# Optimization experiments

Measured on AMD Instinct MI355X. Metric: run time of the kernel, lower is better.

## Reference

```python
import jax, jax.numpy as jnp
import numpy as np

N = 50000      # nodes
E = 1600000    # edges
R = 12         # relations (num_unique_edge_attrs)
F_IN = 64      # num_node_features
H = 128        # hidden_channels
C = 10         # num_classes
G = 256        # graphs in batch
EPS = 1e-5     # BatchNorm eps


def setup_inputs() -> dict:
    key = jax.random.key(0)
    ks = jax.random.split(key, 10)
    s = 0.05
    return {
        "x": jax.random.normal(ks[0], (N, F_IN), jnp.float32),
        "Wrel1": jax.random.normal(ks[1], (R, F_IN, H), jnp.float32) * s,
        "root1": jax.random.normal(ks[2], (F_IN, H), jnp.float32) * s,
        "bias1": jnp.zeros((H,), jnp.float32),
        "gamma1": jnp.ones((H,), jnp.float32),
        "beta1": jnp.zeros((H,), jnp.float32),
        "Wrel2": jax.random.normal(ks[3], (R, H, H), jnp.float32) * s,
        "root2": jax.random.normal(ks[4], (H, H), jnp.float32) * s,
        "bias2": jnp.zeros((H,), jnp.float32),
        "gamma2": jnp.ones((H,), jnp.float32),
        "beta2": jnp.zeros((H,), jnp.float32),
        "Wf": jax.random.normal(ks[5], (H, C), jnp.float32) * s,
        "bf": jnp.zeros((C,), jnp.float32),
        "edge_index": jax.random.randint(ks[6], (2, E), 0, N, dtype=jnp.int64) if jax.config.jax_enable_x64 else jax.random.randint(ks[6], (2, E), 0, N),
        "edge_type": jax.random.randint(ks[7], (E,), 0, R),
        "batch": jnp.sort(jax.random.randint(ks[8], (N,), 0, G)),
    }


def _segment_mean(vals, idx, num):
    # mean aggregation; empty segments -> 0
    s = jax.ops.segment_sum(vals, idx, num_segments=num)
    c = jax.ops.segment_sum(jnp.ones(idx.shape, vals.dtype), idx, num_segments=num)
    return s / jnp.clip(c, 1.0)[:, None]


def _rgcn(x, Wrel, root, bias, src, dst, edge_type):
    # PyG RGCNConv with aggr='mean': per-relation mean of source features, then W_r
    seg = dst * R + edge_type                      # fused (node, relation) segment id
    h = _segment_mean(x[src], seg, N * R)          # [N*R, in]
    h = h.reshape(N, R, x.shape[1])
    return jnp.einsum('nri,rio->no', h, Wrel) + x @ root + bias


def _bn(x, gamma, beta):
    # BatchNorm1d training-mode math (batch statistics, biased variance)
    mu = jnp.mean(x, axis=0)
    var = jnp.mean((x - mu) ** 2, axis=0)
    return gamma * (x - mu) / jnp.sqrt(var + EPS) + beta


def reference(x, Wrel1, root1, bias1, gamma1, beta1,
              Wrel2, root2, bias2, gamma2, beta2,
              Wf, bf, edge_index, edge_type, batch):
    src, dst = edge_index[0], edge_index[1]
    h = jax.nn.relu(_bn(_rgcn(x, Wrel1, root1, bias1, src, dst, edge_type), gamma1, beta1))
    h = jax.nn.relu(_bn(_rgcn(h, Wrel2, root2, bias2, src, dst, edge_type), gamma2, beta2))
    pooled = _segment_mean(h, batch, G)            # global_mean_pool -> [G, H]
    return pooled @ Wf + bf                        # [G, C]
```

## Files before the change

### kernel.cpp

```cpp
#include <hip/hip_runtime.h>

constexpr int N_NODES = 50000;
constexpr int N_EDGES = 1600000;
constexpr int NREL    = 12;
constexpr int F_INPUT = 64;
constexpr int HID     = 128;
constexpr int NCLS    = 10;
constexpr int NGRAPH  = 256;
constexpr int NSEG    = N_NODES * NREL;
constexpr float BN_EPS = 1e-5f;

constexpr int NB    = 391;
constexpr int SEGB  = 128 * NREL;
constexpr int NBLK  = 392;
constexpr int PTPB  = 1024;
constexpr int EPB   = 4096;

typedef float v4f __attribute__((ext_vector_type(4)));
typedef short s8b __attribute__((ext_vector_type(8)));

__device__ __forceinline__ unsigned f2bf(float f) {
    unsigned u = __float_as_uint(f);
    return (u + 0x7FFFu + ((u >> 16) & 1u)) >> 16;
}
__device__ __forceinline__ unsigned pack2(float a, float b) {
    return f2bf(a) | (f2bf(b) << 16);
}

constexpr int PQ0 = 64;
constexpr int PQ1 = PQ0 + 64;
constexpr int PQ2 = PQ1 + 8192;
constexpr int PQ3 = PQ2 + 13 * F_INPUT * HID;
constexpr int PQ4 = PQ3 + 13 * HID * HID;
constexpr int PQ5 = PQ4 + N_NODES * F_INPUT / 4;
constexpr int PQ6 = PQ5 + NGRAPH;
constexpr int PREP_BLOCKS = (PQ6 + 255) / 256;

__global__ void prep(const float* __restrict__ Wrel1, const float* __restrict__ root1,
                     const float* __restrict__ Wrel2, const float* __restrict__ root2,
                     const float* __restrict__ x, const int* __restrict__ batch,
                     ushort* __restrict__ Wp1, ushort* __restrict__ Wp2,
                     ushort* __restrict__ xb,
                     float* __restrict__ bn1, float* __restrict__ bn2,
                     float* __restrict__ psum, float* __restrict__ pcnt) {
    int tid = blockIdx.x * 256 + threadIdx.x;
    const uint4 z = make_uint4(0, 0, 0, 0);
    if (tid < PQ0) { reinterpret_cast<uint4*>(bn1)[tid] = z; return; }
    if (tid < PQ1) { reinterpret_cast<uint4*>(bn2)[tid - PQ0] = z; return; }
    if (tid < PQ2) { reinterpret_cast<uint4*>(psum)[tid - PQ1] = z; return; }
    if (tid < PQ3) {
        int idx = tid - PQ2;
        int r = idx >> 13, rem = idx & 8191;
        int k = rem >> 7, n = rem & 127;
        const float* W = (r < NREL) ? (Wrel1 + (size_t)r * 8192) : root1;
        float v = W[k * HID + n];
        int b = k >> 5, kk = k & 31;
        int j = (n & 7) * 16 + (n >> 3);
        Wp1[(((size_t)(r * 2 + b)) * HID + j) * 32 + kk] = (ushort)f2bf(v);
        return;
    }
    if (tid < PQ4) {
        int idx = tid - PQ3;
        int r = idx >> 14, rem = idx & 16383;
        int k = rem >> 7, n = rem & 127;
        const float* W = (r < NREL) ? (Wrel2 + (size_t)r * 16384) : root2;
        float v = W[k * HID + n];
        int b = k >> 5, kk = k & 31;
        int j = (n & 7) * 16 + (n >> 3);
        Wp2[(((size_t)(r * 4 + b)) * HID + j) * 32 + kk] = (ushort)f2bf(v);
        return;
    }
    if (tid < PQ5) {
        int i = tid - PQ4;
        float4 v = reinterpret_cast<const float4*>(x)[i];
        uint2 o;
        o.x = pack2(v.x, v.y);
        o.y = pack2(v.z, v.w);
        reinterpret_cast<uint2*>(xb)[i] = o;
        return;
    }
    if (tid < PQ6) {
        int g = tid - PQ5;
        int lo0 = 0, hi0 = N_NODES;
        while (lo0 < hi0) { int m = (lo0 + hi0) >> 1; if (batch[m] < g) lo0 = m + 1; else hi0 = m; }
        int lo1 = lo0, hi1 = N_NODES;
        while (lo1 < hi1) { int m = (lo1 + hi1) >> 1; if (batch[m] < g + 1) lo1 = m + 1; else hi1 = m; }
        pcnt[g] = (float)(lo1 - lo0);
    }
}


__global__ __launch_bounds__(PTPB)
void part_hist(const int* __restrict__ dst, int* __restrict__ histG) {
    __shared__ int h[NB];
    int t = threadIdx.x, blk = blockIdx.x;
    if (t < NB) h[t] = 0;
    __syncthreads();
    int base = blk * EPB;
#pragma unroll
    for (int it = 0; it < EPB / PTPB; ++it) {
        int e = base + it * PTPB + t;
        if (e < N_EDGES) atomicAdd(&h[dst[e] >> 7], 1);
    }
    __syncthreads();
    if (t < NB) histG[blk * NB + t] = h[t];
}

__global__ __launch_bounds__(512)
void part_scanA(const int* __restrict__ histG, int* __restrict__ cursorG,
                int* __restrict__ bucketTot) {
    __shared__ int s[512];
    int t = threadIdx.x, b = blockIdx.x;
    int v = (t < NBLK) ? histG[t * NB + b] : 0;
    s[t] = v;
    __syncthreads();
    for (int d = 1; d < 512; d <<= 1) {
        int x = (t >= d) ? s[t - d] : 0;
        __syncthreads();
        s[t] += x;
        __syncthreads();
    }
    if (t < NBLK) cursorG[t * NB + b] = s[t] - v;
    if (t == NBLK - 1) bucketTot[b] = s[t];
}

__global__ __launch_bounds__(512)
void part_scanB(const int* __restrict__ bucketTot, int* __restrict__ bucketBase) {
    __shared__ int s[512];
    int t = threadIdx.x;
    int v = (t < NB) ? bucketTot[t] : 0;
    s[t] = v;
    __syncthreads();
    for (int d = 1; d < 512; d <<= 1) {
        int x = (t >= d) ? s[t - d] : 0;
        __syncthreads();
        s[t] += x;
        __syncthreads();
    }
    if (t <= NB) bucketBase[t] = (t == 0) ? 0 : s[t - 1];
}

__global__ __launch_bounds__(PTPB)
void part_scatter(const int* __restrict__ src, const int* __restrict__ dst,
                  const int* __restrict__ et, const int* __restrict__ cursorG,
                  const int* __restrict__ bucketBase, uint* __restrict__ ebuck) {
    __shared__ int cur[NB];
    int t = threadIdx.x, blk = blockIdx.x;
    if (t < NB) cur[t] = cursorG[blk * NB + t] + bucketBase[t];
    __syncthreads();
    int base = blk * EPB;
#pragma unroll
    for (int it = 0; it < EPB / PTPB; ++it) {
        int e = base + it * PTPB + t;
        if (e < N_EDGES) {
            int d = dst[e];
            int b = d >> 7;
            int pos = atomicAdd(&cur[b], 1);
            ebuck[pos] = (uint)src[e] | ((uint)(d & 127) << 16) | ((uint)et[e] << 23);
        }
    }
}

__global__ __launch_bounds__(256)
void csr_finalize(const uint* __restrict__ ebuck, const int* __restrict__ bucketBase,
                  int* __restrict__ off, int* __restrict__ zrow, float* __restrict__ wgt) {
    __shared__ int cnt[SEGB];
    __shared__ int cur[SEGB];
    __shared__ float winv[SEGB];
    __shared__ int partial[256];
    int t = threadIdx.x, b = blockIdx.x;
    int eb0 = bucketBase[b], eb1 = bucketBase[b + 1];
#pragma unroll
    for (int i = 0; i < 6; ++i) cnt[t * 6 + i] = 0;
    __syncthreads();
    for (int e = eb0 + t; e < eb1; e += 256) {
        uint u = ebuck[e];
        int key = (int)((u >> 16) & 127) * NREL + (int)(u >> 23);
        atomicAdd(&cnt[key], 1);
    }
    __syncthreads();
    int loc[6];
    int sum = 0;
#pragma unroll
    for (int i = 0; i < 6; ++i) { loc[i] = sum; sum += cnt[t * 6 + i]; }
    partial[t] = sum;
    __syncthreads();
    for (int d = 1; d < 256; d <<= 1) {
        int v = (t >= d) ? partial[t - d] : 0;
        __syncthreads();
        partial[t] += v;
        __syncthreads();
    }
    int tbase = (t == 0) ? 0 : partial[t - 1];
    int nodeb = b * 128;
#pragma unroll
    for (int i = 0; i < 6; ++i) {
        int s = t * 6 + i;
        int gpos = eb0 + tbase + loc[i];
        cur[s] = gpos;
        int c = cnt[s];
        winv[s] = (c > 0) ? 1.0f / (float)c : 0.f;
        int node = nodeb + s / NREL;
        if (node < N_NODES) off[node * NREL + (s % NREL)] = gpos;
    }
    __syncthreads();
    for (int e = eb0 + t; e < eb1; e += 256) {
        uint u = ebuck[e];
        int rel = (int)(u >> 23);
        int key = (int)((u >> 16) & 127) * NREL + rel;
        int pos = atomicAdd(&cur[key], 1);
        zrow[pos] = rel * N_NODES + (int)(u & 0xFFFFu);
        wgt[pos] = winv[key];
    }
    if (b == 0 && t == 0) off[NSEG] = N_EDGES;
}


__device__ __constant__ int REL_SPLIT[5] = {0, 4, 7, 10, 13};

template <int F>
__launch_bounds__(256)
__global__ void gemm_rel(const ushort* __restrict__ xin, const ushort* __restrict__ Wp,
                         ushort* __restrict__ Z) {
    constexpr int TN  = 128;
    constexpr int FP2 = F + 8;
    constexpr int KB  = F / 32;
    constexpr int CHW = F / 4;
    constexpr int NLD = CHW / 8;
    __shared__ __align__(16) ushort A[TN * FP2];
    const int t = threadIdx.x;
    const int n0 = blockIdx.x * TN;
    const int r0 = REL_SPLIT[blockIdx.y], r1 = REL_SPLIT[blockIdx.y + 1];
    const int lane = t & 63, wave = t >> 6, q = lane >> 4, l16 = lane & 15;

    {
        const int nl = t >> 2, tid4 = t & 3;
#pragma unroll
        for (int g = 0; g < 2; ++g) {
            int row = g * 64 + nl;
            int n = n0 + row;
            uint4* dstp = reinterpret_cast<uint4*>(A + row * FP2 + tid4 * CHW);
            if (n < N_NODES) {
                const uint4* srcp =
                    reinterpret_cast<const uint4*>(xin + (size_t)n * F + tid4 * CHW);
#pragma unroll
                for (int c = 0; c < NLD; ++c) dstp[c] = srcp[c];
            } else {
                uint4 zz = make_uint4(0, 0, 0, 0);
#pragma unroll
                for (int c = 0; c < NLD; ++c) dstp[c] = zz;
            }
        }
    }
    __syncthreads();

    const int rowbase = wave * 32;
    for (int rel = r0; rel < r1; ++rel) {
        v4f acc[2][8];
#pragma unroll
        for (int st = 0; st < 2; ++st)
#pragma unroll
            for (int nt = 0; nt < 8; ++nt) acc[st][nt] = (v4f){0.f, 0.f, 0.f, 0.f};
#pragma unroll
        for (int b = 0; b < KB; ++b) {
            s8b bfr[8];
            const ushort* wb = Wp + ((size_t)(rel * KB + b) * HID + l16) * 32 + q * 8;
#pragma unroll
            for (int nt = 0; nt < 8; ++nt)
                bfr[nt] = *reinterpret_cast<const s8b*>(wb + (size_t)nt * 16 * 32);
#pragma unroll
            for (int st = 0; st < 2; ++st) {
                s8b af = *reinterpret_cast<const s8b*>(
                    A + (rowbase + st * 16 + l16) * FP2 + b * 32 + q * 8);
#pragma unroll
                for (int nt = 0; nt < 8; ++nt)
                    acc[st][nt] =
                        __builtin_amdgcn_mfma_f32_16x16x32_bf16(af, bfr[nt], acc[st][nt], 0, 0, 0);
            }
        }
        ushort* zr = Z + (size_t)rel * ((size_t)N_NODES * HID);
#pragma unroll
        for (int st = 0; st < 2; ++st) {
            int rowb = n0 + rowbase + st * 16 + q * 4;
#pragma unroll
            for (int rr = 0; rr < 4; ++rr) {
                int n = rowb + rr;
                if (n < N_NODES) {
                    uint4 o;
                    o.x = pack2(acc[st][0][rr], acc[st][1][rr]);
                    o.y = pack2(acc[st][2][rr], acc[st][3][rr]);
                    o.z = pack2(acc[st][4][rr], acc[st][5][rr]);
                    o.w = pack2(acc[st][6][rr], acc[st][7][rr]);
                    *reinterpret_cast<uint4*>(zr + (size_t)n * HID + l16 * 8) = o;
                }
            }
        }
    }
}


__launch_bounds__(256)
__global__ void agg_bn(const ushort* __restrict__ Z, const int* __restrict__ off,
                       const int* __restrict__ zrow, const float* __restrict__ wgt,
                       const float* __restrict__ bias,
                       float* __restrict__ H, float* __restrict__ bn_sum,
                       float* __restrict__ bn_sq) {
    __shared__ float RED[2][4][HID];
    const int t = threadIdx.x;
    const int lane = t & 63, wave = t >> 6;
    const int n0 = blockIdx.x * 32 + wave * 8;
    const float2 bv = *reinterpret_cast<const float2*>(bias + lane * 2);
    float ps0 = 0.f, ps1 = 0.f, pq0 = 0.f, pq1 = 0.f;

    for (int i = 0; i < 8; ++i) {
        int n = n0 + i;
        if (n >= N_NODES) break;
        int e0 = off[n * NREL];
        int ee = off[n * NREL + NREL];
        uint ur = *reinterpret_cast<const uint*>(
            Z + ((size_t)12 * N_NODES + n) * HID + lane * 2);
        float a0 = __uint_as_float(ur << 16) + bv.x;
        float a1 = __uint_as_float(ur & 0xFFFF0000u) + bv.y;
        int elast = ee - 1;
        for (int e = e0; e < ee; e += 8) {
            int zr_[8];
            float w_[8];
#pragma unroll
            for (int j = 0; j < 8; ++j) {
                int ec = min(e + j, elast);
                zr_[j] = zrow[ec];
                w_[j] = (e + j < ee) ? wgt[ec] : 0.f;
            }
            uint u_[8];
#pragma unroll
            for (int j = 0; j < 8; ++j)
                u_[j] = *reinterpret_cast<const uint*>(
                    Z + (size_t)zr_[j] * HID + lane * 2);
#pragma unroll
            for (int j = 0; j < 8; ++j) {
                a0 += __uint_as_float(u_[j] << 16) * w_[j];
                a1 += __uint_as_float(u_[j] & 0xFFFF0000u) * w_[j];
            }
        }
        *reinterpret_cast<float2*>(H + (size_t)n * HID + lane * 2) = make_float2(a0, a1);
        ps0 += a0; ps1 += a1;
        pq0 += a0 * a0; pq1 += a1 * a1;
    }
    RED[0][wave][lane * 2] = ps0; RED[0][wave][lane * 2 + 1] = ps1;
    RED[1][wave][lane * 2] = pq0; RED[1][wave][lane * 2 + 1] = pq1;
    __syncthreads();
    {
        int stat = t >> 7, col = t & 127;
        float v = RED[stat][0][col] + RED[stat][1][col] +
                  RED[stat][2][col] + RED[stat][3][col];
        if (stat == 0) atomicAdd(&bn_sum[col], v);
        else           atomicAdd(&bn_sq[col], v);
    }
}


__global__ void bn_relu_bf16(const float* __restrict__ h, const float* __restrict__ bn_sum,
                             const float* __restrict__ bn_sq, const float* __restrict__ gamma,
                             const float* __restrict__ beta, ushort* __restrict__ outb) {
    __shared__ float CA[HID], CB[HID];
    int t = threadIdx.x;
    if (t < HID) {
        float mu = bn_sum[t] * (1.0f / N_NODES);
        float var = bn_sq[t] * (1.0f / N_NODES) - mu * mu;
        float a = gamma[t] / sqrtf(var + BN_EPS);
        CA[t] = a;
        CB[t] = beta[t] - a * mu;
    }
    __syncthreads();
    int i = blockIdx.x * 256 + t;
    constexpr int TOTAL = N_NODES * HID / 4;
    if (i < TOTAL) {
        int o4 = i & 31;
        float4 a = reinterpret_cast<const float4*>(CA)[o4];
        float4 b = reinterpret_cast<const float4*>(CB)[o4];
        float4 v = reinterpret_cast<const float4*>(h)[i];
        v.x = fmaxf(a.x * v.x + b.x, 0.f);
        v.y = fmaxf(a.y * v.y + b.y, 0.f);
        v.z = fmaxf(a.z * v.z + b.z, 0.f);
        v.w = fmaxf(a.w * v.w + b.w, 0.f);
        uint2 o;
        o.x = pack2(v.x, v.y);
        o.y = pack2(v.z, v.w);
        reinterpret_cast<uint2*>(outb)[i] = o;
    }
}


__global__ void pool_bnrelu(const float* __restrict__ h, const float* __restrict__ bn_sum,
                            const float* __restrict__ bn_sq, const float* __restrict__ gamma,
                            const float* __restrict__ beta, const int* __restrict__ batch,
                            float* __restrict__ psum) {
    __shared__ float CA[HID], CB[HID];
    int t = threadIdx.x;
    if (t < HID) {
        float mu = bn_sum[t] * (1.0f / N_NODES);
        float var = bn_sq[t] * (1.0f / N_NODES) - mu * mu;
        float a = gamma[t] / sqrtf(var + BN_EPS);
        CA[t] = a;
        CB[t] = beta[t] - a * mu;
    }
    __syncthreads();
    int col = t & 127;
    int nb = blockIdx.x * 16 + (t >> 7) * 8;
    float a = CA[col], b = CB[col];
    float run = 0.f;
    int curg = -1;
    for (int i = 0; i < 8; ++i) {
        int n = nb + i;
        if (n < N_NODES) {
            int g = batch[n];
            float v = fmaxf(a * h[(size_t)n * HID + col] + b, 0.f);
            if (g != curg) {
                if (curg >= 0) atomicAdd(&psum[curg * HID + col], run);
                run = 0.f;
                curg = g;
            }
            run += v;
        }
    }
    if (curg >= 0) atomicAdd(&psum[curg * HID + col], run);
}

__global__ void final_kernel(const float* __restrict__ psum, const float* __restrict__ pcnt,
                             const float* __restrict__ Wf, const float* __restrict__ bf,
                             float* __restrict__ out) {
    __shared__ float p[HID];
    int g = blockIdx.x, t = threadIdx.x;
    float inv = 1.0f / fmaxf(pcnt[g], 1.0f);
    p[t] = psum[g * HID + t] * inv;
    p[t + 64] = psum[g * HID + t + 64] * inv;
    __syncthreads();
    if (t < NCLS) {
        float s = bf[t];
#pragma unroll 16
        for (int k = 0; k < HID; ++k) s += p[k] * Wf[k * NCLS + t];
        out[g * NCLS + t] = s;
    }
}


extern "C" void kernel_launch(void* const* d_in, const int* in_sizes, int n_in,
                              void* d_out, int out_size, void* d_ws, size_t ws_size,
                              hipStream_t stream) {
    const float* x      = (const float*)d_in[0];
    const float* Wrel1  = (const float*)d_in[1];
    const float* root1  = (const float*)d_in[2];
    const float* bias1  = (const float*)d_in[3];
    const float* gamma1 = (const float*)d_in[4];
    const float* beta1  = (const float*)d_in[5];
    const float* Wrel2  = (const float*)d_in[6];
    const float* root2  = (const float*)d_in[7];
    const float* bias2  = (const float*)d_in[8];
    const float* gamma2 = (const float*)d_in[9];
    const float* beta2  = (const float*)d_in[10];
    const float* Wf     = (const float*)d_in[11];
    const float* bf     = (const float*)d_in[12];
    const int* ei       = (const int*)d_in[13];
    const int* et       = (const int*)d_in[14];
    const int* batch    = (const int*)d_in[15];
    const int* srcv = ei;
    const int* dstv = ei + N_EDGES;

    char* w = (char*)d_ws;
    auto alloc = [&](size_t bytes) -> char* {
        char* p = w;
        w += (bytes + 255) / 256 * 256;
        return p;
    };
    int* off     = (int*)alloc((size_t)(NSEG + 1) * 4);
    int* zrow    = (int*)alloc((size_t)N_EDGES * 4);
    float* wgt   = (float*)alloc((size_t)N_EDGES * 4);
    ushort* xb   = (ushort*)alloc((size_t)N_NODES * F_INPUT * 2);
    ushort* H1b  = (ushort*)alloc((size_t)N_NODES * HID * 2);
    ushort* Wp1  = (ushort*)alloc((size_t)13 * F_INPUT * HID * 2);
    ushort* Wp2  = (ushort*)alloc((size_t)13 * HID * HID * 2);
    float* bn1   = (float*)alloc(2 * HID * 4);
    float* bn2   = (float*)alloc(2 * HID * 4);
    float* psum  = (float*)alloc((size_t)NGRAPH * HID * 4);
    float* pcnt  = (float*)alloc((size_t)NGRAPH * 4);
    float* Hbuf  = (float*)alloc((size_t)N_NODES * HID * 4);
    char* ovl    = alloc((size_t)13 * N_NODES * HID * 2);
    int* histG      = (int*)ovl;
    int* cursorG    = (int*)(ovl + (size_t)NBLK * NB * 4);
    int* bucketTot  = (int*)(ovl + (size_t)2 * NBLK * NB * 4);
    int* bucketBase = (int*)(ovl + (size_t)2 * NBLK * NB * 4 + (NB + 1) * 4 + 252);
    uint* ebuck     = (uint*)(ovl + (size_t)2 * NBLK * NB * 4 + 4096);
    ushort* Zb      = (ushort*)ovl;

    prep<<<PREP_BLOCKS, 256, 0, stream>>>(Wrel1, root1, Wrel2, root2, x, batch,
                                          Wp1, Wp2, xb, bn1, bn2, psum, pcnt);

    part_hist<<<NBLK, PTPB, 0, stream>>>(dstv, histG);
    part_scanA<<<NB, 512, 0, stream>>>(histG, cursorG, bucketTot);
    part_scanB<<<1, 512, 0, stream>>>(bucketTot, bucketBase);
    part_scatter<<<NBLK, PTPB, 0, stream>>>(srcv, dstv, et, cursorG, bucketBase, ebuck);
    csr_finalize<<<NB, 256, 0, stream>>>(ebuck, bucketBase, off, zrow, wgt);

    dim3 ggrid((N_NODES + 127) / 128, 4);
    int ablk = (N_NODES + 31) / 32;

    gemm_rel<F_INPUT><<<ggrid, 256, 0, stream>>>(xb, Wp1, Zb);
    agg_bn<<<ablk, 256, 0, stream>>>(Zb, off, zrow, wgt, bias1, Hbuf, bn1, bn1 + HID);
    bn_relu_bf16<<<(N_NODES * HID / 4 + 255) / 256, 256, 0, stream>>>(Hbuf, bn1, bn1 + HID,
                                                                      gamma1, beta1, H1b);

    gemm_rel<HID><<<ggrid, 256, 0, stream>>>(H1b, Wp2, Zb);
    agg_bn<<<ablk, 256, 0, stream>>>(Zb, off, zrow, wgt, bias2, Hbuf, bn2, bn2 + HID);

    pool_bnrelu<<<(N_NODES + 15) / 16, 256, 0, stream>>>(Hbuf, bn2, bn2 + HID, gamma2, beta2,
                                                         batch, psum);
    final_kernel<<<NGRAPH, 64, 0, stream>>>(psum, pcnt, Wf, bf, (float*)d_out);
}
```

Measured before the change: 492.2 us.

## Aggregate-then-transform for layer 1 via per-relation mean and concatenated GEMM

For the first RGCN layer, the order of operations is swapped: the per-relation mean of 64-wide bf16 source features is computed first into a concatenated [N, 13*64] buffer (including the root self features). A single GEMM against the stacked weights then fuses bias and the BatchNorm statistic reductions. This avoids materializing and gathering the 13x128-wide transformed Z tensor, shrinking the gather width from 128 to 64. The cost is an extra esrc array written in CSR finalize and an intermediate M buffer round-trip.

```diff
diff --git a/kernel.cpp b/kernel.cpp
--- a/kernel.cpp
+++ b/kernel.cpp
@@ -163,7 +163,8 @@
 
 __global__ __launch_bounds__(256)
 void csr_finalize(const uint* __restrict__ ebuck, const int* __restrict__ bucketBase,
-                  int* __restrict__ off, int* __restrict__ zrow, float* __restrict__ wgt) {
+                  int* __restrict__ off, int* __restrict__ esrc,
+                  int* __restrict__ zrow, float* __restrict__ wgt) {
     __shared__ int cnt[SEGB];
     __shared__ int cur[SEGB];
     __shared__ float winv[SEGB];
@@ -209,10 +210,154 @@
         int rel = (int)(u >> 23);
         int key = (int)((u >> 16) & 127) * NREL + rel;
         int pos = atomicAdd(&cur[key], 1);
-        zrow[pos] = rel * N_NODES + (int)(u & 0xFFFFu);
+        int srcn = (int)(u & 0xFFFFu);
+        esrc[pos] = srcn;
+        zrow[pos] = rel * N_NODES + srcn;
         wgt[pos] = winv[key];
     }
     if (b == 0 && t == 0) off[NSEG] = N_EDGES;
+}
+
+
+template <int F>
+__launch_bounds__(256)
+__global__ void agg_m(const ushort* __restrict__ xin, const int* __restrict__ off,
+                      const int* __restrict__ esrc, ushort* __restrict__ Mb) {
+    constexpr int KT = 13 * F;
+    const int t = threadIdx.x;
+    const int lane = t & 63, wave = t >> 6;
+    const int half = lane >> 5;
+    const int cofs = (F == 128) ? lane * 2 : (lane & 31) * 2;
+    const int n0 = blockIdx.x * 32 + wave * 8;
+
+    for (int i = 0; i < 8; ++i) {
+        int n = n0 + i;
+        if (n >= N_NODES) break;
+        if (F == 128 || half == 0) {
+            uint ur = *reinterpret_cast<const uint*>(xin + (size_t)n * F + cofs);
+            *reinterpret_cast<uint*>(Mb + (size_t)n * KT + 12 * F + cofs) = ur;
+        }
+        constexpr int NR = (F == 128) ? 12 : 6;
+#pragma unroll 2
+        for (int rr = 0; rr < NR; ++rr) {
+            int r = (F == 128) ? rr : rr * 2 + half;
+            int e0 = off[n * NREL + r], e1 = off[n * NREL + r + 1];
+            float f0 = 0.f, f1 = 0.f;
+            int elast = e1 - 1;
+            for (int e = e0; e < e1; e += 4) {
+                int i0 = esrc[e];
+                int i1 = esrc[min(e + 1, elast)];
+                int i2 = esrc[min(e + 2, elast)];
+                int i3 = esrc[min(e + 3, elast)];
+                uint u0 = *reinterpret_cast<const uint*>(xin + (size_t)i0 * F + cofs);
+                uint u1 = *reinterpret_cast<const uint*>(xin + (size_t)i1 * F + cofs);
+                uint u2 = *reinterpret_cast<const uint*>(xin + (size_t)i2 * F + cofs);
+                uint u3 = *reinterpret_cast<const uint*>(xin + (size_t)i3 * F + cofs);
+                f0 += __uint_as_float(u0 << 16);
+                f1 += __uint_as_float(u0 & 0xFFFF0000u);
+                if (e + 1 < e1) { f0 += __uint_as_float(u1 << 16); f1 += __uint_as_float(u1 & 0xFFFF0000u); }
+                if (e + 2 < e1) { f0 += __uint_as_float(u2 << 16); f1 += __uint_as_float(u2 & 0xFFFF0000u); }
+                if (e + 3 < e1) { f0 += __uint_as_float(u3 << 16); f1 += __uint_as_float(u3 & 0xFFFF0000u); }
+            }
+            if (e1 > e0) {
+                float inv = 1.0f / (float)(e1 - e0);
+                f0 *= inv; f1 *= inv;
+            }
+            *reinterpret_cast<uint*>(Mb + (size_t)n * KT + r * F + cofs) = pack2(f0, f1);
+        }
+    }
+}
+
+
+template <int F>
+__launch_bounds__(256)
+__global__ void gemm_cat(const ushort* __restrict__ Mb, const ushort* __restrict__ Wp,
+                         const float* __restrict__ bias, float* __restrict__ H,
+                         float* __restrict__ bn_sum, float* __restrict__ bn_sq) {
+    constexpr int KT  = 13 * F;
+    constexpr int NCH = KT / 64;
+    __shared__ __align__(16) ushort As[64 * 72];
+    const int t = threadIdx.x;
+    const int n0 = blockIdx.x * 64;
+    const int lane = t & 63, wave = t >> 6, q = lane >> 4, l16 = lane & 15;
+    const int srow = t >> 2, sq = t & 3;
+    const int nstage = n0 + srow;
+
+    v4f acc[8];
+#pragma unroll
+    for (int nt = 0; nt < 8; ++nt) acc[nt] = (v4f){0.f, 0.f, 0.f, 0.f};
+
+    for (int c = 0; c < NCH; ++c) {
+        __syncthreads();
+        {
+            uint4 v0 = make_uint4(0, 0, 0, 0), v1 = v0;
+            if (nstage < N_NODES) {
+                const uint4* sp = reinterpret_cast<const uint4*>(
+                    Mb + (size_t)nstage * KT + c * 64 + sq * 16);
+                v0 = sp[0];
+                v1 = sp[1];
+            }
+            uint4* dp = reinterpret_cast<uint4*>(As + srow * 72 + sq * 16);
+            dp[0] = v0;
+            dp[1] = v1;
+        }
+        __syncthreads();
+#pragma unroll
+        for (int b = 0; b < 2; ++b) {
+            const int kbg = c * 2 + b;
+            const ushort* wb = Wp + ((size_t)kbg * HID + l16) * 32 + q * 8;
+            s8b af = *reinterpret_cast<const s8b*>(As + (wave * 16 + l16) * 72 + b * 32 + q * 8);
+#pragma unroll
+            for (int nt = 0; nt < 8; ++nt) {
+                s8b bfb = *reinterpret_cast<const s8b*>(wb + (size_t)nt * 16 * 32);
+                acc[nt] = __builtin_amdgcn_mfma_f32_16x16x32_bf16(af, bfb, acc[nt], 0, 0, 0);
+            }
+        }
+    }
+
+    __syncthreads();
+    float* REDs = reinterpret_cast<float*>(As);
+    float* REDq = REDs + 512;
+    const int colb = l16 * 8;
+    float4 b0 = *reinterpret_cast<const float4*>(bias + colb);
+    float4 b1 = *reinterpret_cast<const float4*>(bias + colb + 4);
+    float s_[8] = {0, 0, 0, 0, 0, 0, 0, 0}, q2_[8] = {0, 0, 0, 0, 0, 0, 0, 0};
+#pragma unroll
+    for (int rr = 0; rr < 4; ++rr) {
+        int n = n0 + wave * 16 + q * 4 + rr;
+        if (n < N_NODES) {
+            float v0 = acc[0][rr] + b0.x, v1 = acc[1][rr] + b0.y;
+            float v2 = acc[2][rr] + b0.z, v3 = acc[3][rr] + b0.w;
+            float v4 = acc[4][rr] + b1.x, v5 = acc[5][rr] + b1.y;
+            float v6 = acc[6][rr] + b1.z, v7 = acc[7][rr] + b1.w;
+            *reinterpret_cast<float4*>(H + (size_t)n * HID + colb) = make_float4(v0, v1, v2, v3);
+            *reinterpret_cast<float4*>(H + (size_t)n * HID + colb + 4) = make_float4(v4, v5, v6, v7);
+            s_[0] += v0; s_[1] += v1; s_[2] += v2; s_[3] += v3;
+            s_[4] += v4; s_[5] += v5; s_[6] += v6; s_[7] += v7;
+            q2_[0] += v0 * v0; q2_[1] += v1 * v1; q2_[2] += v2 * v2; q2_[3] += v3 * v3;
+            q2_[4] += v4 * v4; q2_[5] += v5 * v5; q2_[6] += v6 * v6; q2_[7] += v7 * v7;
+        }
+    }
+#pragma unroll
+    for (int nt = 0; nt < 8; ++nt) {
+        s_[nt] += __shfl_xor(s_[nt], 16);  s_[nt] += __shfl_xor(s_[nt], 32);
+        q2_[nt] += __shfl_xor(q2_[nt], 16); q2_[nt] += __shfl_xor(q2_[nt], 32);
+    }
+    if (lane < 16) {
+#pragma unroll
+        for (int nt = 0; nt < 8; ++nt) {
+            REDs[wave * 128 + colb + nt] = s_[nt];
+            REDq[wave * 128 + colb + nt] = q2_[nt];
+        }
+    }
+    __syncthreads();
+    {
+        int stat = t >> 7, col = t & 127;
+        const float* R = stat ? REDq : REDs;
+        float v = R[0 * 128 + col] + R[1 * 128 + col] + R[2 * 128 + col] + R[3 * 128 + col];
+        if (stat == 0) atomicAdd(&bn_sum[col], v);
+        else           atomicAdd(&bn_sq[col], v);
+    }
 }
 
 
@@ -473,6 +618,7 @@
         return p;
     };
     int* off     = (int*)alloc((size_t)(NSEG + 1) * 4);
+    int* esrc    = (int*)alloc((size_t)N_EDGES * 4);
     int* zrow    = (int*)alloc((size_t)N_EDGES * 4);
     float* wgt   = (float*)alloc((size_t)N_EDGES * 4);
     ushort* xb   = (ushort*)alloc((size_t)N_NODES * F_INPUT * 2);
@@ -490,6 +636,7 @@
     int* bucketTot  = (int*)(ovl + (size_t)2 * NBLK * NB * 4);
     int* bucketBase = (int*)(ovl + (size_t)2 * NBLK * NB * 4 + (NB + 1) * 4 + 252);
     uint* ebuck     = (uint*)(ovl + (size_t)2 * NBLK * NB * 4 + 4096);
+    ushort* Mbuf    = (ushort*)ovl;
     ushort* Zb      = (ushort*)ovl;
 
     prep<<<PREP_BLOCKS, 256, 0, stream>>>(Wrel1, root1, Wrel2, root2, x, batch,
@@ -499,13 +646,14 @@
     part_scanA<<<NB, 512, 0, stream>>>(histG, cursorG, bucketTot);
     part_scanB<<<1, 512, 0, stream>>>(bucketTot, bucketBase);
     part_scatter<<<NBLK, PTPB, 0, stream>>>(srcv, dstv, et, cursorG, bucketBase, ebuck);
-    csr_finalize<<<NB, 256, 0, stream>>>(ebuck, bucketBase, off, zrow, wgt);
-
+    csr_finalize<<<NB, 256, 0, stream>>>(ebuck, bucketBase, off, esrc, zrow, wgt);
+
+    int ablk = (N_NODES + 31) / 32;
+    int gcblk = (N_NODES + 63) / 64;
     dim3 ggrid((N_NODES + 127) / 128, 4);
-    int ablk = (N_NODES + 31) / 32;
-
-    gemm_rel<F_INPUT><<<ggrid, 256, 0, stream>>>(xb, Wp1, Zb);
-    agg_bn<<<ablk, 256, 0, stream>>>(Zb, off, zrow, wgt, bias1, Hbuf, bn1, bn1 + HID);
+
+    agg_m<F_INPUT><<<ablk, 256, 0, stream>>>(xb, off, esrc, Mbuf);
+    gemm_cat<F_INPUT><<<gcblk, 256, 0, stream>>>(Mbuf, Wp1, bias1, Hbuf, bn1, bn1 + HID);
     bn_relu_bf16<<<(N_NODES * HID / 4 + 255) / 256, 256, 0, stream>>>(Hbuf, bn1, bn1 + HID,
                                                                       gamma1, beta1, H1b);
 
```

Result: slower. 504.4 us (+2.5%).
